# Optimization experiments

Hardware: AMD Instinct MI355X
Metric: run time of the kernel (lower is better)

Reference implementation:

```python
import jax, jax.numpy as jnp
import numpy as np

HIDDEN = 2048
NUM_HEADS = 8
NUM_KV_HEADS = 2
HEAD_DIM = 256
ROPE_BASE = 1e6
EPS = 1e-6
B, S = 2, 2048


def rms_norm(x, w, eps=EPS):
    # normalize over last dim (head_dim), per-head
    var = jnp.mean(jnp.square(x), axis=-1, keepdims=True)
    return x * jax.lax.rsqrt(var + eps) * w


def rope(x, positions, base=ROPE_BASE):
    # neox-style rotate-half RoPE over full head_dim. x: [B,S,H,D], positions: [B,S]
    d = x.shape[-1]
    inv_freq = 1.0 / (base ** (jnp.arange(0, d, 2, dtype=jnp.float32) / d))
    freqs = positions.astype(jnp.float32)[..., None] * inv_freq  # [B,S,D/2]
    cos = jnp.cos(freqs)[:, :, None, :]
    sin = jnp.sin(freqs)[:, :, None, :]
    x1, x2 = x[..., : d // 2], x[..., d // 2 :]
    return jnp.concatenate([x1 * cos - x2 * sin, x2 * cos + x1 * sin], axis=-1)


def setup_inputs() -> dict:
    key = jax.random.key(0)
    k1, k2, k3 = jax.random.split(key, 3)
    hidden_states = jax.random.normal(k1, (B, S, HIDDEN), dtype=jnp.float32)
    positions = jnp.broadcast_to(jnp.arange(S, dtype=jnp.int32), (B, S))
    qkv_out = (NUM_HEADS + 2 * NUM_KV_HEADS) * HEAD_DIM
    w_qkv = jax.random.normal(k2, (HIDDEN, qkv_out), dtype=jnp.float32) * (HIDDEN ** -0.5)
    w_o = jax.random.normal(k3, (NUM_HEADS * HEAD_DIM, HIDDEN), dtype=jnp.float32) * ((NUM_HEADS * HEAD_DIM) ** -0.5)
    q_norm_w = jnp.ones((HEAD_DIM,), dtype=jnp.float32)
    k_norm_w = jnp.ones((HEAD_DIM,), dtype=jnp.float32)
    return {"hidden_states": hidden_states, "positions": positions, "w_qkv": w_qkv,
            "w_o": w_o, "q_norm_w": q_norm_w, "k_norm_w": k_norm_w}


def reference(hidden_states, positions, w_qkv, w_o, q_norm_w, k_norm_w):
    b, s, _ = hidden_states.shape
    q_size = NUM_HEADS * HEAD_DIM
    kv_size = NUM_KV_HEADS * HEAD_DIM
    qkv = hidden_states @ w_qkv  # [B,S,q+2kv]
    q, k, v = jnp.split(qkv, [q_size, q_size + kv_size], axis=-1)
    q = q.reshape(b, s, NUM_HEADS, HEAD_DIM)
    k = k.reshape(b, s, NUM_KV_HEADS, HEAD_DIM)
    v = v.reshape(b, s, NUM_KV_HEADS, HEAD_DIM)
    # per-head RMSNorm; v_norm has no learned scale (weight fixed to ones)
    q = rms_norm(q, q_norm_w)
    k = rms_norm(k, k_norm_w)
    v = rms_norm(v, jnp.ones((HEAD_DIM,), dtype=v.dtype))
    # RoPE
    q = rope(q, positions)
    k = rope(k, positions)
    # GQA: repeat kv heads
    g = NUM_HEADS // NUM_KV_HEADS
    k = jnp.repeat(k, g, axis=2)
    v = jnp.repeat(v, g, axis=2)
    # causal attention with scaling = 1.0 (as in module)
    scores = jnp.einsum("bqhd,bkhd->bhqk", q, k)
    mask = jnp.tril(jnp.ones((s, s), dtype=bool))
    scores = jnp.where(mask, scores, jnp.finfo(scores.dtype).min)
    probs = jax.nn.softmax(scores, axis=-1)
    attn = jnp.einsum("bhqk,bkhd->bqhd", probs, v).reshape(b, s, NUM_HEADS * HEAD_DIM)
    return attn @ w_o
```

## Files before the change

kernel.cpp:

```cpp
#include <hip/hip_runtime.h>


#define HID  2048
#define NH   8
#define NKV  2
#define HD   256
#define SB   2048
#define BB   2
#define MTOK (BB * SB)
#define NQKV ((NH + 2 * NKV) * HD)

typedef _Float16  f16x8 __attribute__((ext_vector_type(8)));
typedef float     f32x4 __attribute__((ext_vector_type(4)));

__device__ __forceinline__ unsigned short f2h(float f) {
  _Float16 h = (_Float16)f;
  return __builtin_bit_cast(unsigned short, h);
}

__device__ __forceinline__ void async_copy16(const unsigned short* g, unsigned short* l) {
  __builtin_amdgcn_global_load_lds(
      (const __attribute__((address_space(1))) unsigned int*)g,
      (__attribute__((address_space(3))) unsigned int*)l, 16, 0, 0);
}

__device__ __forceinline__ int swz4(int r) { return (r + (r >> 2)) & 3; }

template <int OUT_MODE>
__global__ __launch_bounds__(256) void gemm_bt(const unsigned short* __restrict__ A,
                                               const unsigned short* __restrict__ Bt,
                                               void* __restrict__ Cg,
                                               int M, int N, int K) {
  __shared__ unsigned short Ash[128 * 32];
  __shared__ unsigned short Bsh[128 * 32];
  const int t = threadIdx.x;
  const int lane = t & 63, w = t >> 6;
  const int quad = lane >> 4, m15 = lane & 15;
  const int wm = w >> 1, wn = w & 1;
  const int m0 = blockIdx.y * 128, n0 = blockIdx.x * 128;

  const int rowS0 = t >> 2, rowS1 = rowS0 + 64;
  const int slot = t & 3;
  const int g0 = (slot ^ swz4(rowS0)) * 8;
  const int g1 = (slot ^ swz4(rowS1)) * 8;
  const unsigned short* Ag0 = A + (size_t)(m0 + rowS0) * K + g0;
  const unsigned short* Ag1 = A + (size_t)(m0 + rowS1) * K + g1;
  const unsigned short* Bg0 = Bt + (size_t)(n0 + rowS0) * K + g0;
  const unsigned short* Bg1 = Bt + (size_t)(n0 + rowS1) * K + g1;
  unsigned short* lA0 = &Ash[t * 8];
  unsigned short* lA1 = &Ash[(t + 256) * 8];
  unsigned short* lB0 = &Bsh[t * 8];
  unsigned short* lB1 = &Bsh[(t + 256) * 8];

  int offA[4], offB[4];
#pragma unroll
  for (int i = 0; i < 4; ++i) {
    const int ra = wm * 64 + i * 16 + m15;
    offA[i] = ra * 32 + (quad ^ swz4(ra)) * 8;
    const int rb = wn * 64 + i * 16 + m15;
    offB[i] = rb * 32 + (quad ^ swz4(rb)) * 8;
  }

  const f32x4 vz = {0.f, 0.f, 0.f, 0.f};
  f32x4 acc[4][4];
#pragma unroll
  for (int i = 0; i < 4; ++i)
#pragma unroll
    for (int j = 0; j < 4; ++j) acc[i][j] = vz;

  const int nk = K >> 5;
  for (int kt = 0; kt < nk; ++kt) {
    const int k0 = kt * 32;
    async_copy16(Ag0 + k0, lA0);
    async_copy16(Ag1 + k0, lA1);
    async_copy16(Bg0 + k0, lB0);
    async_copy16(Bg1 + k0, lB1);
    __syncthreads();
    f16x8 af[4], bfr[4];
#pragma unroll
    for (int i = 0; i < 4; ++i) af[i] = *(const f16x8*)&Ash[offA[i]];
#pragma unroll
    for (int j = 0; j < 4; ++j) bfr[j] = *(const f16x8*)&Bsh[offB[j]];
#pragma unroll
    for (int i = 0; i < 4; ++i)
#pragma unroll
      for (int j = 0; j < 4; ++j)
        acc[i][j] = __builtin_amdgcn_mfma_f32_16x16x32_f16(af[i], bfr[j], acc[i][j], 0, 0, 0);
    __syncthreads();
  }

#pragma unroll
  for (int i = 0; i < 4; ++i)
#pragma unroll
    for (int j = 0; j < 4; ++j)
#pragma unroll
      for (int r = 0; r < 4; ++r) {
        const int gm = m0 + wm * 64 + i * 16 + quad * 4 + r;
        const int gn = n0 + wn * 64 + j * 16 + m15;
        const float v = acc[i][j][r];
        if (OUT_MODE == 2) ((float*)Cg)[(size_t)gm * N + gn] = v;
        else               ((unsigned short*)Cg)[(size_t)gm * N + gn] = f2h(v);
      }
}

__global__ __launch_bounds__(256) void cvt_f32_f16(const float* __restrict__ in,
                                                   unsigned short* __restrict__ out, int n4) {
  const int i = blockIdx.x * 256 + threadIdx.x;
  if (i >= n4) return;
  const float4 v = ((const float4*)in)[i];
  ushort4 o = {f2h(v.x), f2h(v.y), f2h(v.z), f2h(v.w)};
  ((ushort4*)out)[i] = o;
}

__global__ __launch_bounds__(256) void transpose_f2h(const float* __restrict__ in,
                                                     unsigned short* __restrict__ out,
                                                     int R, int C) {
  __shared__ float tile[64 * 68];
  const int r0 = blockIdx.y * 64, c0 = blockIdx.x * 64;
  const int t = threadIdx.x;
#pragma unroll
  for (int p = 0; p < 4; ++p) {
    const int idx = t + p * 256;
    const int rr = idx >> 4, cc = (idx & 15) * 4;
    *(float4*)&tile[rr * 68 + cc] = *(const float4*)&in[(size_t)(r0 + rr) * C + c0 + cc];
  }
  __syncthreads();
#pragma unroll
  for (int p = 0; p < 2; ++p) {
    const int idx = t + p * 256;
    const int dr = idx >> 3, sc = (idx & 7) * 8;
    union { uint4 v; unsigned short s[8]; } o;
#pragma unroll
    for (int e = 0; e < 8; ++e) o.s[e] = f2h(tile[(sc + e) * 68 + dr]);
    *(uint4*)&out[(size_t)(c0 + dr) * R + r0 + sc] = o.v;
  }
}

__global__ __launch_bounds__(256) void normrope(const unsigned short* __restrict__ qkv,
                                                const int* __restrict__ pos,
                                                const float* __restrict__ qw,
                                                const float* __restrict__ kw,
                                                unsigned short* __restrict__ Qh,
                                                unsigned short* __restrict__ Kh,
                                                unsigned short* __restrict__ Vh) {
  const int tok = blockIdx.x;
  const int b = tok >> 11, s = tok & 2047;
  const int t = threadIdx.x, w = t >> 6, lane = t & 63;
  const float p = (float)pos[tok];
  const int dbase = lane * 4;

  for (int it = 0; it < 3; ++it) {
    const int slot = it * 4 + w;
    const unsigned short* src = qkv + (size_t)tok * NQKV + slot * 256 + dbase;
    union { uint2 u; _Float16 h[4]; } rd;
    rd.u = *(const uint2*)src;
    float y[4];
#pragma unroll
    for (int e = 0; e < 4; ++e) y[e] = (float)rd.h[e];
    float ssq = y[0] * y[0] + y[1] * y[1] + y[2] * y[2] + y[3] * y[3];
#pragma unroll
    for (int off = 1; off < 64; off <<= 1) ssq += __shfl_xor(ssq, off);
    const float rn = rsqrtf(ssq * (1.f / 256.f) + 1e-6f);

    if (slot < 8) {
#pragma unroll
      for (int e = 0; e < 4; ++e) y[e] *= rn * qw[dbase + e];
    } else if (slot < 10) {
#pragma unroll
      for (int e = 0; e < 4; ++e) y[e] *= rn * kw[dbase + e];
    } else {
#pragma unroll
      for (int e = 0; e < 4; ++e) y[e] *= rn;
    }

    unsigned short* dst;
    if (slot < 8)       dst = Qh + ((size_t)(b * NH + slot) * SB + s) * HD + dbase;
    else if (slot < 10) dst = Kh + ((size_t)(b * NKV + slot - 8) * SB + s) * HD + dbase;
    else                dst = Vh + ((size_t)(b * NKV + slot - 10) * SB + s) * HD + dbase;

    float outv[4];
    if (slot < 10) {
      const int i0 = dbase & 127;
      const bool lo = (lane < 32);
#pragma unroll
      for (int e = 0; e < 4; ++e) {
        const float partner = __shfl_xor(y[e], 32);
        const float invf = expf(-(float)(i0 + e) * 0.10793368f);
        const float fr = p * invf;
        const float cv = cosf(fr), sv = sinf(fr);
        outv[e] = lo ? (y[e] * cv - partner * sv) : (y[e] * cv + partner * sv);
      }
    } else {
#pragma unroll
      for (int e = 0; e < 4; ++e) outv[e] = y[e];
    }
    union { uint2 u; _Float16 h[4]; } wr;
#pragma unroll
    for (int e = 0; e < 4; ++e) wr.h[e] = (_Float16)outv[e];
    *(uint2*)dst = wr.u;
  }
}

__global__ __launch_bounds__(256) void transpose_u16(const unsigned short* __restrict__ in,
                                                     unsigned short* __restrict__ out,
                                                     int R, int C, size_t ibs, size_t obs) {
  __shared__ unsigned short tile[64 * 72];
  const unsigned short* ib = in + blockIdx.z * ibs;
  unsigned short* ob = out + blockIdx.z * obs;
  const int r0 = blockIdx.y * 64, c0 = blockIdx.x * 64;
  const int t = threadIdx.x;
#pragma unroll
  for (int pck = 0; pck < 2; ++pck) {
    const int c = t + pck * 256;
    const int rr = c >> 3, cc = (c & 7) * 8;
    *(uint4*)&tile[rr * 72 + cc] = *(const uint4*)&ib[(size_t)(r0 + rr) * C + c0 + cc];
  }
  __syncthreads();
#pragma unroll
  for (int pck = 0; pck < 2; ++pck) {
    const int c = t + pck * 256;
    const int dr = c >> 3, sc = (c & 7) * 8;
    union { uint4 v; unsigned short s[8]; } o;
#pragma unroll
    for (int e = 0; e < 8; ++e) o.s[e] = tile[(sc + e) * 72 + dr];
    *(uint4*)&ob[(size_t)(c0 + dr) * R + r0 + sc] = o.v;
  }
}

__global__ __launch_bounds__(512, 2) void flash_attn(const unsigned short* __restrict__ Qh,
                                                     const unsigned short* __restrict__ Kh,
                                                     const unsigned short* __restrict__ Vt,
                                                     unsigned short* __restrict__ attn) {
  __shared__ __align__(16) unsigned char SMEM[142336];
  unsigned short* Ksh = (unsigned short*)SMEM;
  unsigned short* Vsh = (unsigned short*)(SMEM + 65536);
  _Float16*      Psh  = (_Float16*)(SMEM + 131072);
  float*         MLx  = (float*)(SMEM + 141312);
  float*         mergeO = (float*)SMEM;

  const int pairi = blockIdx.x;
  const int h = blockIdx.y, b = blockIdx.z;
  const int kv = h >> 2;
  const int t = threadIdx.x, w = t >> 6, lane = t & 63;
  const int wq = w & 3, team = w >> 2;
  const int quad = lane >> 4, m15 = lane & 15;

  const unsigned short* Kb = Kh + (size_t)(b * NKV + kv) * SB * HD;
  const unsigned short* Vb = Vt + (size_t)(b * NKV + kv) * HD * SB;

  const int krow = t >> 5, kchunk = t & 31;
  const int vrow = t >> 3, vchunk = t & 7;

  const f32x4 vz = {0.f, 0.f, 0.f, 0.f};

  for (int jb = 0; jb < 2; ++jb) {
    const int qt = jb ? (31 - pairi) : pairi;
    const int q0 = qt * 64, qw0 = q0 + wq * 16;

    f16x8 aq[8];
    const unsigned short* qb = Qh + ((size_t)(b * NH + h) * SB + qw0 + m15) * HD + quad * 8;
#pragma unroll
    for (int ks = 0; ks < 8; ++ks) aq[ks] = *(const f16x8*)(qb + ks * 32);

    f32x4 o[16];
#pragma unroll
    for (int i = 0; i < 16; ++i) o[i] = vz;
    float mrow[4] = {-1e30f, -1e30f, -1e30f, -1e30f};
    float lrow[4] = {0.f, 0.f, 0.f, 0.f};

    const int nkt = (q0 + 64) >> 6;

#pragma unroll
    for (int shot = 0; shot < 4; ++shot) {
      const int r = krow + 16 * shot;
      async_copy16(Kb + (size_t)r * HD + ((kchunk ^ (r & 7)) * 8),
                   &Ksh[4096 * shot + t * 8]);
    }
#pragma unroll
    for (int shot = 0; shot < 4; ++shot) {
      const int d = vrow + 64 * shot;
      async_copy16(Vb + (size_t)d * SB + ((vchunk ^ (d & 7)) * 8),
                   &Vsh[4096 * shot + t * 8]);
    }
    __syncthreads();

    for (int kt = 0; kt < nkt; ++kt) {
      const int k0 = kt * 64;
      const int par = kt & 1;

      if (kt + 1 < nkt) {
        const int kn = k0 + 64;
        const int pn = par ^ 1;
#pragma unroll
        for (int shot = 0; shot < 4; ++shot) {
          const int r = krow + 16 * shot;
          async_copy16(Kb + (size_t)(kn + r) * HD + ((kchunk ^ (r & 7)) * 8),
                       &Ksh[pn * 16384 + 4096 * shot + t * 8]);
        }
#pragma unroll
        for (int shot = 0; shot < 4; ++shot) {
          const int d = vrow + 64 * shot;
          async_copy16(Vb + (size_t)d * SB + kn + ((vchunk ^ (d & 7)) * 8),
                       &Vsh[pn * 16384 + 4096 * shot + t * 8]);
        }
      }

      const unsigned short* KB = &Ksh[par * 16384];
      const unsigned short* VB = &Vsh[par * 16384];

      f32x4 sv[2];
      sv[0] = vz; sv[1] = vz;
#pragma unroll
      for (int g = 0; g < 2; ++g) {
        const int key = team * 32 + g * 16 + m15;
        const unsigned short* kr = &KB[key * 256];
        const int sw = (key & 7);
#pragma unroll
        for (int ks = 0; ks < 8; ++ks) {
          const f16x8 bk = *(const f16x8*)&kr[((4 * ks + quad) ^ sw) * 8];
          sv[g] = __builtin_amdgcn_mfma_f32_16x16x32_f16(aq[ks], bk, sv[g], 0, 0, 0);
        }
      }

      const bool last = (kt == nkt - 1);
#pragma unroll
      for (int r = 0; r < 4; ++r) {
        const int q = qw0 + quad * 4 + r;
        float s[2];
#pragma unroll
        for (int g = 0; g < 2; ++g) {
          s[g] = sv[g][r];
          if (last && (k0 + team * 32 + g * 16 + m15) > q) s[g] = -3.0e38f;
        }
        float tm = fmaxf(s[0], s[1]);
#pragma unroll
        for (int off = 1; off < 16; off <<= 1) tm = fmaxf(tm, __shfl_xor(tm, off));
        const float mnew = fmaxf(mrow[r], tm);
        const float alpha = __expf(mrow[r] - mnew);
        float p[2], rs;
        p[0] = __expf(s[0] - mnew);
        p[1] = __expf(s[1] - mnew);
        rs = p[0] + p[1];
#pragma unroll
        for (int off = 1; off < 16; off <<= 1) rs += __shfl_xor(rs, off);
        lrow[r] = lrow[r] * alpha + rs;
        mrow[r] = mnew;
#pragma unroll
        for (int dbi = 0; dbi < 16; ++dbi) o[dbi][r] *= alpha;
        _Float16* pr = &Psh[w * 640 + (quad * 4 + r) * 40];
        const int wx = quad << 3;
        pr[(m15) ^ wx]      = (_Float16)p[0];
        pr[(16 + m15) ^ wx] = (_Float16)p[1];
      }

      asm volatile("" ::: "memory");
      {
        const f16x8 ap = *(const f16x8*)&Psh[w * 640 + m15 * 40 + ((quad ^ (m15 >> 2)) << 3)];
#pragma unroll
        for (int dbi = 0; dbi < 16; ++dbi) {
          const int d = dbi * 16 + m15;
          const f16x8 bv = *(const f16x8*)&VB[d * 64 + (((team * 4 + quad) ^ (d & 7)) * 8)];
          o[dbi] = __builtin_amdgcn_mfma_f32_16x16x32_f16(ap, bv, o[dbi], 0, 0, 0);
        }
      }

      __syncthreads();
    }

    if (m15 == 0) {
#pragma unroll
      for (int r = 0; r < 4; ++r) {
        MLx[w * 32 + (quad * 4 + r) * 2]     = mrow[r];
        MLx[w * 32 + (quad * 4 + r) * 2 + 1] = lrow[r];
      }
    }
    {
      float* mo = mergeO + w * 2080;
#pragma unroll
      for (int ii = 0; ii < 8; ++ii) {
        const int i = team ? ii : (8 + ii);
        const int dcol = ii * 16 + m15;
#pragma unroll
        for (int r = 0; r < 4; ++r) mo[(quad * 4 + r) * 130 + dcol] = o[i][r];
      }
    }
    __syncthreads();
    {
      const int pw = w ^ 4;
      const float* pmo = mergeO + pw * 2080;
#pragma unroll
      for (int r = 0; r < 4; ++r) {
        const int row = quad * 4 + r;
        const int q = qw0 + row;
        const float pm = MLx[pw * 32 + row * 2];
        const float pl = MLx[pw * 32 + row * 2 + 1];
        const float m = fmaxf(mrow[r], pm);
        const float a0 = __expf(mrow[r] - m);
        const float a1 = __expf(pm - m);
        const float invl = 1.0f / (a0 * lrow[r] + a1 * pl);
#pragma unroll
        for (int ii = 0; ii < 8; ++ii) {
          const int i = team ? (8 + ii) : ii;
          const float po = pmo[row * 130 + ii * 16 + m15];
          const float val = (a0 * o[i][r] + a1 * po) * invl;
          const int col = h * HD + team * 128 + ii * 16 + m15;
          attn[(size_t)(b * SB + q) * (NH * HD) + col] = f2h(val);
        }
      }
    }
    __syncthreads();
  }
}

static constexpr size_t OFF_HB   = 0;
static constexpr size_t OFF_QH   = 0;
static constexpr size_t OFF_W1T  = 16777216;
static constexpr size_t OFF_KH   = 16777216;
static constexpr size_t OFF_VH   = 20971520;
static constexpr size_t OFF_VT   = 25165824;
static constexpr size_t OFF_WOT  = 29360128;
static constexpr size_t OFF_QKV  = 37748736;
static constexpr size_t OFF_ATTN = OFF_QKV;

extern "C" void kernel_launch(void* const* d_in, const int* in_sizes, int n_in,
                              void* d_out, int out_size, void* d_ws, size_t ws_size,
                              hipStream_t stream) {
  const float* hidden    = (const float*)d_in[0];
  const int*   positions = (const int*)d_in[1];
  const float* w_qkv     = (const float*)d_in[2];
  const float* w_o       = (const float*)d_in[3];
  const float* qw        = (const float*)d_in[4];
  const float* kw        = (const float*)d_in[5];
  float* out = (float*)d_out;
  char* ws = (char*)d_ws;

  unsigned short* hb    = (unsigned short*)(ws + OFF_HB);
  unsigned short* wqkvT = (unsigned short*)(ws + OFF_W1T);
  unsigned short* woT   = (unsigned short*)(ws + OFF_WOT);
  unsigned short* qkvb  = (unsigned short*)(ws + OFF_QKV);
  unsigned short* attnb = (unsigned short*)(ws + OFF_ATTN);
  unsigned short* Qhb   = (unsigned short*)(ws + OFF_QH);
  unsigned short* Khb   = (unsigned short*)(ws + OFF_KH);
  unsigned short* Vhb   = (unsigned short*)(ws + OFF_VH);
  unsigned short* Vtb   = (unsigned short*)(ws + OFF_VT);

  cvt_f32_f16<<<dim3((MTOK * HID / 4 + 255) / 256), 256, 0, stream>>>(hidden, hb, MTOK * HID / 4);
  transpose_f2h<<<dim3(NQKV / 64, HID / 64), 256, 0, stream>>>(w_qkv, wqkvT, HID, NQKV);
  transpose_f2h<<<dim3(HID / 64, HID / 64), 256, 0, stream>>>(w_o, woT, HID, HID);

  gemm_bt<0><<<dim3(NQKV / 128, MTOK / 128), 256, 0, stream>>>(hb, wqkvT, qkvb, MTOK, NQKV, HID);

  normrope<<<dim3(MTOK), 256, 0, stream>>>(qkvb, positions, qw, kw, Qhb, Khb, Vhb);

  transpose_u16<<<dim3(HD / 64, SB / 64, BB * NKV), 256, 0, stream>>>(Vhb, Vtb, SB, HD,
                                                                     (size_t)SB * HD, (size_t)SB * HD);

  flash_attn<<<dim3(16, NH, BB), 512, 0, stream>>>(Qhb, Khb, Vtb, attnb);

  gemm_bt<2><<<dim3(HID / 128, MTOK / 128), 256, 0, stream>>>(attnb, woT, out, MTOK, HID, HID);
}
```

Before: 362.4 us.

## Compute transposed attention tiles to keep P in registers and skip LDS

Swaps the MFMA operand order so scores come out transposed, with each lane owning one query row. The softmax probabilities can then be packed straight into the B operand of the PV MFMA, with no LDS round trip. V rows are written in permuted order during normrope so the key ordering matches the register layout of P. The rescale of O and l is skipped when no lane's max increases (checked with __all), and the output merge writes 4 halves per store. The added risk is that the V permutation must exactly match the MFMA fragment layout, and it ties the normrope output to flash_attn's internal tiling.

```diff
diff --git a/kernel.cpp b/kernel.cpp
--- a/kernel.cpp
+++ b/kernel.cpp
@@ -148,6 +148,8 @@
   const int t = threadIdx.x, w = t >> 6, lane = t & 63;
   const float p = (float)pos[tok];
   const int dbase = lane * 4;
+  const int s5 = s & 31;
+  const int sp = (s & ~31) | (((s5 >> 2) & 3) << 3) | (((s5 >> 4) & 1) << 2) | (s5 & 3);
 
   for (int it = 0; it < 3; ++it) {
     const int slot = it * 4 + w;
@@ -176,7 +178,7 @@
     unsigned short* dst;
     if (slot < 8)       dst = Qh + ((size_t)(b * NH + slot) * SB + s) * HD + dbase;
     else if (slot < 10) dst = Kh + ((size_t)(b * NKV + slot - 8) * SB + s) * HD + dbase;
-    else                dst = Vh + ((size_t)(b * NKV + slot - 10) * SB + s) * HD + dbase;
+    else                dst = Vh + ((size_t)(b * NKV + slot - 10) * SB + sp) * HD + dbase;
 
     float outv[4];
     if (slot < 10) {
@@ -231,11 +233,10 @@
                                                      const unsigned short* __restrict__ Kh,
                                                      const unsigned short* __restrict__ Vt,
                                                      unsigned short* __restrict__ attn) {
-  __shared__ __align__(16) unsigned char SMEM[142336];
+  __shared__ __align__(16) unsigned char SMEM[132096];
   unsigned short* Ksh = (unsigned short*)SMEM;
   unsigned short* Vsh = (unsigned short*)(SMEM + 65536);
-  _Float16*      Psh  = (_Float16*)(SMEM + 131072);
-  float*         MLx  = (float*)(SMEM + 141312);
+  float*         MLx  = (float*)(SMEM + 131072);
   float*         mergeO = (float*)SMEM;
 
   const int pairi = blockIdx.x;
@@ -256,6 +257,7 @@
   for (int jb = 0; jb < 2; ++jb) {
     const int qt = jb ? (31 - pairi) : pairi;
     const int q0 = qt * 64, qw0 = q0 + wq * 16;
+    const int qlane = qw0 + m15;
 
     f16x8 aq[8];
     const unsigned short* qb = Qh + ((size_t)(b * NH + h) * SB + qw0 + m15) * HD + quad * 8;
@@ -265,8 +267,7 @@
     f32x4 o[16];
 #pragma unroll
     for (int i = 0; i < 16; ++i) o[i] = vz;
-    float mrow[4] = {-1e30f, -1e30f, -1e30f, -1e30f};
-    float lrow[4] = {0.f, 0.f, 0.f, 0.f};
+    float mrow = -1e30f, lrow = 0.f;
 
     const int nkt = (q0 + 64) >> 6;
 
@@ -317,95 +318,94 @@
         const int sw = (key & 7);
 #pragma unroll
         for (int ks = 0; ks < 8; ++ks) {
-          const f16x8 bk = *(const f16x8*)&kr[((4 * ks + quad) ^ sw) * 8];
-          sv[g] = __builtin_amdgcn_mfma_f32_16x16x32_f16(aq[ks], bk, sv[g], 0, 0, 0);
+          const f16x8 ak = *(const f16x8*)&kr[((4 * ks + quad) ^ sw) * 8];
+          sv[g] = __builtin_amdgcn_mfma_f32_16x16x32_f16(ak, aq[ks], sv[g], 0, 0, 0);
         }
       }
 
       const bool last = (kt == nkt - 1);
-#pragma unroll
-      for (int r = 0; r < 4; ++r) {
-        const int q = qw0 + quad * 4 + r;
-        float s[2];
-#pragma unroll
-        for (int g = 0; g < 2; ++g) {
-          s[g] = sv[g][r];
-          if (last && (k0 + team * 32 + g * 16 + m15) > q) s[g] = -3.0e38f;
+      float p2[2][4];
+#pragma unroll
+      for (int g = 0; g < 2; ++g)
+#pragma unroll
+        for (int r = 0; r < 4; ++r) {
+          float s = sv[g][r];
+          if (last && (k0 + team * 32 + g * 16 + quad * 4 + r) > qlane) s = -3.0e38f;
+          p2[g][r] = s;
         }
-        float tm = fmaxf(s[0], s[1]);
-#pragma unroll
-        for (int off = 1; off < 16; off <<= 1) tm = fmaxf(tm, __shfl_xor(tm, off));
-        const float mnew = fmaxf(mrow[r], tm);
-        const float alpha = __expf(mrow[r] - mnew);
-        float p[2], rs;
-        p[0] = __expf(s[0] - mnew);
-        p[1] = __expf(s[1] - mnew);
-        rs = p[0] + p[1];
-#pragma unroll
-        for (int off = 1; off < 16; off <<= 1) rs += __shfl_xor(rs, off);
-        lrow[r] = lrow[r] * alpha + rs;
-        mrow[r] = mnew;
-#pragma unroll
-        for (int dbi = 0; dbi < 16; ++dbi) o[dbi][r] *= alpha;
-        _Float16* pr = &Psh[w * 640 + (quad * 4 + r) * 40];
-        const int wx = quad << 3;
-        pr[(m15) ^ wx]      = (_Float16)p[0];
-        pr[(16 + m15) ^ wx] = (_Float16)p[1];
-      }
-
-      asm volatile("" ::: "memory");
-      {
-        const f16x8 ap = *(const f16x8*)&Psh[w * 640 + m15 * 40 + ((quad ^ (m15 >> 2)) << 3)];
-#pragma unroll
-        for (int dbi = 0; dbi < 16; ++dbi) {
-          const int d = dbi * 16 + m15;
-          const f16x8 bv = *(const f16x8*)&VB[d * 64 + (((team * 4 + quad) ^ (d & 7)) * 8)];
-          o[dbi] = __builtin_amdgcn_mfma_f32_16x16x32_f16(ap, bv, o[dbi], 0, 0, 0);
-        }
+      float tm = fmaxf(fmaxf(fmaxf(p2[0][0], p2[0][1]), fmaxf(p2[0][2], p2[0][3])),
+                       fmaxf(fmaxf(p2[1][0], p2[1][1]), fmaxf(p2[1][2], p2[1][3])));
+      tm = fmaxf(tm, __shfl_xor(tm, 16));
+      tm = fmaxf(tm, __shfl_xor(tm, 32));
+      if (!__all(tm <= mrow)) {
+        const float mnew = fmaxf(mrow, tm);
+        const float alpha = __expf(mrow - mnew);
+        lrow *= alpha;
+#pragma unroll
+        for (int dbi = 0; dbi < 16; ++dbi) o[dbi] *= alpha;
+        mrow = mnew;
+      }
+      float rs = 0.f;
+#pragma unroll
+      for (int g = 0; g < 2; ++g)
+#pragma unroll
+        for (int r = 0; r < 4; ++r) { p2[g][r] = __expf(p2[g][r] - mrow); rs += p2[g][r]; }
+      rs += __shfl_xor(rs, 16);
+      rs += __shfl_xor(rs, 32);
+      lrow += rs;
+
+      f16x8 bp;
+#pragma unroll
+      for (int g = 0; g < 2; ++g)
+#pragma unroll
+        for (int r = 0; r < 4; ++r) bp[g * 4 + r] = (_Float16)p2[g][r];
+
+#pragma unroll
+      for (int dbi = 0; dbi < 16; ++dbi) {
+        const int d = dbi * 16 + m15;
+        const f16x8 av = *(const f16x8*)&VB[d * 64 + (((team * 4 + quad) ^ (d & 7)) * 8)];
+        o[dbi] = __builtin_amdgcn_mfma_f32_16x16x32_f16(av, bp, o[dbi], 0, 0, 0);
       }
 
       __syncthreads();
     }
 
-    if (m15 == 0) {
-#pragma unroll
-      for (int r = 0; r < 4; ++r) {
-        MLx[w * 32 + (quad * 4 + r) * 2]     = mrow[r];
-        MLx[w * 32 + (quad * 4 + r) * 2 + 1] = lrow[r];
-      }
+    if (quad == 0) {
+      MLx[w * 32 + m15 * 2]     = mrow;
+      MLx[w * 32 + m15 * 2 + 1] = lrow;
     }
     {
-      float* mo = mergeO + w * 2080;
+      float* mo = mergeO + w * 2176;
 #pragma unroll
       for (int ii = 0; ii < 8; ++ii) {
-        const int i = team ? ii : (8 + ii);
-        const int dcol = ii * 16 + m15;
-#pragma unroll
-        for (int r = 0; r < 4; ++r) mo[(quad * 4 + r) * 130 + dcol] = o[i][r];
+        const int dbi = team ? ii : (8 + ii);
+#pragma unroll
+        for (int r = 0; r < 4; ++r)
+          mo[(ii * 16 + quad * 4 + r) * 17 + m15] = o[dbi][r];
       }
     }
     __syncthreads();
     {
       const int pw = w ^ 4;
-      const float* pmo = mergeO + pw * 2080;
-#pragma unroll
-      for (int r = 0; r < 4; ++r) {
-        const int row = quad * 4 + r;
-        const int q = qw0 + row;
-        const float pm = MLx[pw * 32 + row * 2];
-        const float pl = MLx[pw * 32 + row * 2 + 1];
-        const float m = fmaxf(mrow[r], pm);
-        const float a0 = __expf(mrow[r] - m);
-        const float a1 = __expf(pm - m);
-        const float invl = 1.0f / (a0 * lrow[r] + a1 * pl);
-#pragma unroll
-        for (int ii = 0; ii < 8; ++ii) {
-          const int i = team ? (8 + ii) : ii;
-          const float po = pmo[row * 130 + ii * 16 + m15];
-          const float val = (a0 * o[i][r] + a1 * po) * invl;
-          const int col = h * HD + team * 128 + ii * 16 + m15;
-          attn[(size_t)(b * SB + q) * (NH * HD) + col] = f2h(val);
+      const float* pmo = mergeO + pw * 2176;
+      const float pm = MLx[pw * 32 + m15 * 2];
+      const float pl = MLx[pw * 32 + m15 * 2 + 1];
+      const float mm = fmaxf(mrow, pm);
+      const float a0 = __expf(mrow - mm);
+      const float a1 = __expf(pm - mm);
+      const float invl = 1.0f / (a0 * lrow + a1 * pl);
+      const int q = qlane;
+#pragma unroll
+      for (int ii = 0; ii < 8; ++ii) {
+        const int dbi = team ? (8 + ii) : ii;
+        union { uint2 u; _Float16 hh[4]; } st;
+#pragma unroll
+        for (int r = 0; r < 4; ++r) {
+          const float po = pmo[(ii * 16 + quad * 4 + r) * 17 + m15];
+          st.hh[r] = (_Float16)((a0 * o[dbi][r] + a1 * po) * invl);
         }
+        const int dcol = team * 128 + ii * 16 + quad * 4;
+        *(uint2*)&attn[(size_t)(b * SB + q) * (NH * HD) + h * HD + dcol] = st.u;
       }
     }
     __syncthreads();
```

Result: faster. 343.9 us (-5.1%).
